# Kernel tuning notes

Measured on AMD Instinct MI355X. Metric: run time of the kernel, lower is better.

Reference implementation:

```python
import jax, jax.numpy as jnp
import numpy as np

T, N, E, D = 4, 50000, 800000, 256
VOCAB = 64000


def _gcn_layer(x, row, col, w, W, b, n):
    # PyG GCNConv: add self-loops (weight 1), symmetric normalization on
    # weighted in-degree (target/col), h = x @ W, scatter-add, then + bias.
    loops = jnp.arange(n, dtype=row.dtype)
    row2 = jnp.concatenate([row, loops])
    col2 = jnp.concatenate([col, loops])
    w2 = jnp.concatenate([w, jnp.ones((n,), x.dtype)])
    deg = jax.ops.segment_sum(w2, col2, num_segments=n)
    dinv = jnp.where(deg > 0, jax.lax.rsqrt(deg), 0.0)
    norm = dinv[row2] * w2 * dinv[col2]              # [E+N]
    h = x @ W                                        # [N, D]
    out = jax.ops.segment_sum(norm[:, None] * h[row2], col2, num_segments=n)
    return out + b


def _encode_timestep(ids, row, col, w, emb, W1, b1, W2, b2, W3, b3):
    x = emb[ids]                                     # [N, D] embedding lookup
    x = _gcn_layer(x, row, col, w, W1, b1, ids.shape[0])
    x = _gcn_layer(x, row, col, w, W2, b2, ids.shape[0])
    x = _gcn_layer(x, row, col, w, W3, b3, ids.shape[0])
    return x


def setup_inputs() -> dict:
    key = jax.random.key(0)
    ks = jax.random.split(key, 8)
    scale = 1.0 / np.sqrt(D)
    return {
        "node_features": jax.random.randint(ks[0], (T, N), 0, VOCAB, dtype=jnp.int32),
        "edge_index": jax.random.randint(ks[1], (T, 2, E), 0, N, dtype=jnp.int32),
        "edge_weight": jax.random.uniform(ks[2], (T, E), dtype=jnp.float32),
        "emb": jax.random.normal(ks[3], (VOCAB, D), dtype=jnp.float32),
        "W1": jax.random.normal(ks[4], (D, D), dtype=jnp.float32) * scale,
        "b1": jnp.zeros((D,), jnp.float32),
        "W2": jax.random.normal(ks[5], (D, D), dtype=jnp.float32) * scale,
        "b2": jnp.zeros((D,), jnp.float32),
        "W3": jax.random.normal(ks[6], (D, D), dtype=jnp.float32) * scale,
        "b3": jnp.zeros((D,), jnp.float32),
    }


def reference(node_features, edge_index, edge_weight, emb, W1, b1, W2, b2, W3, b3):
    outs = []
    for t in range(node_features.shape[0]):  # fixed small timestep count
        outs.append(_encode_timestep(node_features[t], edge_index[t, 0],
                                     edge_index[t, 1], edge_weight[t],
                                     emb, W1, b1, W2, b2, W3, b3))
    return jnp.concatenate(outs, axis=0)  # [T*N, D]
```

## Files before the change

kernel.cpp:

```cpp
#include <hip/hip_runtime.h>

#define T_STEPS 4
#define NN 50000
#define EE 800000
#define DD 256
#define NB ((NN + 255) / 256)

typedef __attribute__((ext_vector_type(8))) short short8;
typedef __attribute__((ext_vector_type(4))) float floatx4;

__device__ __forceinline__ unsigned short f2bf(float f) {
    unsigned u = __float_as_uint(f);
    return (unsigned short)((u + 0x7FFFu + ((u >> 16) & 1u)) >> 16);
}
__device__ __forceinline__ float bf2f(unsigned short s) {
    return __uint_as_float(((unsigned)s) << 16);
}

__device__ __forceinline__ void async16(const unsigned short* g, unsigned short* l) {
    __builtin_amdgcn_global_load_lds(
        (const __attribute__((address_space(1))) void*)g,
        (__attribute__((address_space(3))) void*)l, 16, 0, 0);
}

__global__ __launch_bounds__(256) void init_deg_cnt(float* __restrict__ deg,
                                                    int* __restrict__ cnt, int n) {
    int i = blockIdx.x * 256 + threadIdx.x;
    if (i < n) { deg[i] = 1.0f; cnt[i] = 0; }
}

__global__ __launch_bounds__(256) void edge_deg_cnt(const int* __restrict__ col,
                                                    const float* __restrict__ w,
                                                    float* __restrict__ deg,
                                                    int* __restrict__ cnt, int e) {
    int i = blockIdx.x * 256 + threadIdx.x;
    if (i < e) {
        int c = col[i];
        atomicAdd(&deg[c], w[i]);
        atomicAdd(&cnt[c], 1);
    }
}

__global__ __launch_bounds__(256) void compute_dinv(const float* __restrict__ deg,
                                                    float* __restrict__ dinv, int n) {
    int i = blockIdx.x * 256 + threadIdx.x;
    if (i < n) {
        float d = deg[i];
        dinv[i] = d > 0.0f ? rsqrtf(d) : 0.0f;
    }
}

__global__ __launch_bounds__(256) void block_sums(const int* __restrict__ cnt,
                                                  int* __restrict__ bsum, int n) {
    __shared__ int sm[256];
    int i = blockIdx.x * 256 + threadIdx.x;
    sm[threadIdx.x] = (i < n) ? cnt[i] : 0;
    __syncthreads();
    for (int s = 128; s > 0; s >>= 1) {
        if ((int)threadIdx.x < s) sm[threadIdx.x] += sm[threadIdx.x + s];
        __syncthreads();
    }
    if (threadIdx.x == 0) bsum[blockIdx.x] = sm[0];
}

__global__ __launch_bounds__(256) void scan_bsum(const int* __restrict__ bsum,
                                                 int* __restrict__ boff, int nb) {
    __shared__ int sm[256];
    int v = ((int)threadIdx.x < nb) ? bsum[threadIdx.x] : 0;
    sm[threadIdx.x] = v;
    __syncthreads();
    for (int o = 1; o < 256; o <<= 1) {
        int t = (threadIdx.x >= (unsigned)o) ? sm[threadIdx.x - o] : 0;
        __syncthreads();
        sm[threadIdx.x] += t;
        __syncthreads();
    }
    if ((int)threadIdx.x < nb) boff[threadIdx.x] = sm[threadIdx.x] - v;
}

__global__ __launch_bounds__(256) void scan_final(const int* __restrict__ cnt,
                                                  const int* __restrict__ boff,
                                                  int* __restrict__ colptr,
                                                  int* __restrict__ next, int n, int e) {
    __shared__ int sm[256];
    int i = blockIdx.x * 256 + threadIdx.x;
    int v = (i < n) ? cnt[i] : 0;
    sm[threadIdx.x] = v;
    __syncthreads();
    for (int o = 1; o < 256; o <<= 1) {
        int t = (threadIdx.x >= (unsigned)o) ? sm[threadIdx.x - o] : 0;
        __syncthreads();
        sm[threadIdx.x] += t;
        __syncthreads();
    }
    int excl = sm[threadIdx.x] - v + boff[blockIdx.x];
    if (i < n) { colptr[i] = excl; next[i] = excl; }
    if (i == 0) colptr[n] = e;
}

__global__ __launch_bounds__(256) void fill_csr(const int* __restrict__ row,
                                                const int* __restrict__ col,
                                                const float* __restrict__ w,
                                                const float* __restrict__ dinv,
                                                int* __restrict__ next,
                                                int* __restrict__ srow,
                                                float* __restrict__ snorm, int e) {
    int i = blockIdx.x * 256 + threadIdx.x;
    if (i < e) {
        int r = row[i], c = col[i];
        int p = atomicAdd(&next[c], 1);
        srow[p] = r;
        snorm[p] = dinv[r] * w[i] * dinv[c];
    }
}

__global__ __launch_bounds__(256) void convert_w(const float* __restrict__ W0,
                                                 const float* __restrict__ W1,
                                                 const float* __restrict__ W2,
                                                 unsigned short* __restrict__ wt) {
    int n = blockIdx.x;
    int k = threadIdx.x;
    int l = blockIdx.y;
    const float* W = (l == 0) ? W0 : (l == 1) ? W1 : W2;
    wt[(size_t)l * 65536 + n * 256 + k] = f2bf(W[k * 256 + n]);
}

__global__ __launch_bounds__(256) void embed_kernel(const int* __restrict__ ids,
                                                    const float* __restrict__ emb,
                                                    unsigned short* __restrict__ xb,
                                                    int n) {
    int t = blockIdx.x * 256 + threadIdx.x;
    if (t < n * 64) {
        int node = t >> 6;
        int j = t & 63;
        float4 v = ((const float4*)emb)[(size_t)ids[node] * 64 + j];
        ushort4 o;
        o.x = f2bf(v.x); o.y = f2bf(v.y); o.z = f2bf(v.z); o.w = f2bf(v.w);
        ((ushort4*)xb)[(size_t)node * 64 + j] = o;
    }
}

__global__ __launch_bounds__(256) void mfma_gemm(const unsigned short* __restrict__ xb,
                                                 const unsigned short* __restrict__ wt,
                                                 unsigned short* __restrict__ h2,
                                                 int M) {
    __shared__ __align__(16) unsigned short As[128 * 32];
    __shared__ __align__(16) unsigned short Bs[128 * 32];

    int tid = threadIdx.x;
    int lane = tid & 63;
    int wave = tid >> 6;
    int row0 = blockIdx.y * 128;
    int col0 = blockIdx.x * 128;
    int wm = (wave & 1) * 64;
    int wn = (wave >> 1) * 64;
    int quad = lane >> 4;
    int cl = lane & 15;

    int idx0 = tid, idx1 = 256 + tid;
    int c0 = idx0 >> 7, m0 = idx0 & 127;
    int c1 = idx1 >> 7, m1 = idx1 & 127;
    int gr0 = row0 + m0; if (gr0 >= M) gr0 = M - 1;
    int gr1 = row0 + m1; if (gr1 >= M) gr1 = M - 1;
    const unsigned short* srcA0 = xb + (size_t)gr0 * 256 + c0 * 8;
    const unsigned short* srcA1 = xb + (size_t)gr1 * 256 + c1 * 8;
    const unsigned short* srcB0 = wt + (size_t)(col0 + m0) * 256 + c0 * 8;
    const unsigned short* srcB1 = wt + (size_t)(col0 + m1) * 256 + c1 * 8;
    unsigned short* dstA0 = As + idx0 * 8;
    unsigned short* dstA1 = As + idx1 * 8;
    unsigned short* dstB0 = Bs + idx0 * 8;
    unsigned short* dstB1 = Bs + idx1 * 8;

    floatx4 acc[4][4] = {};

    for (int k0 = 0; k0 < 256; k0 += 32) {
        if (k0) __syncthreads();
        async16(srcA0 + k0, dstA0);
        async16(srcA1 + k0, dstA1);
        async16(srcB0 + k0, dstB0);
        async16(srcB1 + k0, dstB1);
        __syncthreads();

        short8 af[4], bfr[4];
#pragma unroll
        for (int i = 0; i < 4; ++i)
            af[i] = *(const short8*)&As[(quad * 128 + wm + i * 16 + cl) * 8];
#pragma unroll
        for (int j = 0; j < 4; ++j)
            bfr[j] = *(const short8*)&Bs[(quad * 128 + wn + j * 16 + cl) * 8];
#pragma unroll
        for (int i = 0; i < 4; ++i)
#pragma unroll
            for (int j = 0; j < 4; ++j)
                acc[i][j] = __builtin_amdgcn_mfma_f32_16x16x32_bf16(
                    af[i], bfr[j], acc[i][j], 0, 0, 0);
    }

#pragma unroll
    for (int i = 0; i < 4; ++i) {
#pragma unroll
        for (int r = 0; r < 4; ++r) {
            int gr = row0 + wm + i * 16 + quad * 4 + r;
            if (gr < M) {
                size_t base = (size_t)gr * 256 + col0 + wn + cl;
#pragma unroll
                for (int j = 0; j < 4; ++j)
                    h2[base + j * 16] = f2bf(acc[i][j][r]);
            }
        }
    }
}

__global__ __launch_bounds__(256) void agg_kernel(const unsigned short* __restrict__ h2,
                                                  const int* __restrict__ colptr,
                                                  const int* __restrict__ srow,
                                                  const float* __restrict__ snorm,
                                                  const float* __restrict__ dinv,
                                                  const float* __restrict__ bias,
                                                  float* __restrict__ dstf,
                                                  unsigned short* __restrict__ dstb,
                                                  int n) {
    int wave = threadIdx.x >> 6;
    int lane = threadIdx.x & 63;
    int c = blockIdx.x * 4 + wave;
    if (c >= n) return;
    int p0 = colptr[c];
    int p1 = colptr[c + 1];
    float di = dinv[c];
    float self = di * di;

    const ushort4* h4 = (const ushort4*)h2;
    int cbase = c * 64 + lane;

    ushort4 sv = h4[cbase];
    float ax = self * bf2f(sv.x), ay = self * bf2f(sv.y);
    float az = self * bf2f(sv.z), aw = self * bf2f(sv.w);
    float bx = 0.f, by = 0.f, bz = 0.f, bw = 0.f;

    int j = p0;
    for (; j + 1 < p1; j += 2) {
        int r0 = srow[j];
        int r1 = srow[j + 1];
        float w0 = snorm[j];
        float w1 = snorm[j + 1];
        ushort4 v0 = h4[(size_t)r0 * 64 + lane];
        ushort4 v1 = h4[(size_t)r1 * 64 + lane];
        ax += w0 * bf2f(v0.x); ay += w0 * bf2f(v0.y);
        az += w0 * bf2f(v0.z); aw += w0 * bf2f(v0.w);
        bx += w1 * bf2f(v1.x); by += w1 * bf2f(v1.y);
        bz += w1 * bf2f(v1.z); bw += w1 * bf2f(v1.w);
    }
    if (j < p1) {
        int r0 = srow[j];
        float w0 = snorm[j];
        ushort4 v0 = h4[(size_t)r0 * 64 + lane];
        ax += w0 * bf2f(v0.x); ay += w0 * bf2f(v0.y);
        az += w0 * bf2f(v0.z); aw += w0 * bf2f(v0.w);
    }
    float4 bv = ((const float4*)bias)[lane];
    float ox = ax + bx + bv.x, oy = ay + by + bv.y;
    float oz = az + bz + bv.z, ow = aw + bw + bv.w;
    if (dstb) {
        ushort4 o;
        o.x = f2bf(ox); o.y = f2bf(oy); o.z = f2bf(oz); o.w = f2bf(ow);
        ((ushort4*)dstb)[cbase] = o;
    } else {
        ((float4*)dstf)[cbase] = make_float4(ox, oy, oz, ow);
    }
}

extern "C" void kernel_launch(void* const* d_in, const int* in_sizes, int n_in,
                              void* d_out, int out_size, void* d_ws, size_t ws_size,
                              hipStream_t stream) {
    const int*   node_features = (const int*)d_in[0];
    const int*   edge_index    = (const int*)d_in[1];
    const float* edge_weight   = (const float*)d_in[2];
    const float* emb           = (const float*)d_in[3];
    const float* Wl[3] = {(const float*)d_in[4], (const float*)d_in[6], (const float*)d_in[8]};
    const float* bl[3] = {(const float*)d_in[5], (const float*)d_in[7], (const float*)d_in[9]};
    float* out = (float*)d_out;

    char* ws = (char*)d_ws;
    size_t off = 0;
    auto alloc = [&](size_t bytes) -> void* {
        void* p = ws + off;
        off = (off + bytes + 255) & ~(size_t)255;
        return p;
    };
    unsigned short* xb     = (unsigned short*)alloc((size_t)NN * DD * 2);
    unsigned short* h2     = (unsigned short*)alloc((size_t)NN * DD * 2);
    unsigned short* wt     = (unsigned short*)alloc((size_t)3 * DD * DD * 2);
    float* deg    = (float*)alloc((size_t)NN * 4);
    float* dinv   = (float*)alloc((size_t)NN * 4);
    int*   cnt    = (int*)alloc((size_t)NN * 4);
    int*   colptr = (int*)alloc((size_t)(NN + 1) * 4);
    int*   next   = (int*)alloc((size_t)NN * 4);
    int*   srow   = (int*)alloc((size_t)EE * 4);
    float* snorm  = (float*)alloc((size_t)EE * 4);
    int*   bsum   = (int*)alloc((size_t)NB * 4);
    int*   boff   = (int*)alloc((size_t)NB * 4);
    (void)ws_size; (void)n_in; (void)in_sizes; (void)out_size;

    const int gN   = (NN + 255) / 256;
    const int gE   = (EE + 255) / 256;
    const int gX   = (NN * 64 + 255) / 256;
    const int gAgg = (NN + 3) / 4;
    dim3 gGemm(2, (NN + 127) / 128);
    dim3 gCvt(256, 3);

    convert_w<<<gCvt, 256, 0, stream>>>(Wl[0], Wl[1], Wl[2], wt);

    for (int t = 0; t < T_STEPS; ++t) {
        const int*   ids = node_features + (size_t)t * NN;
        const int*   row = edge_index + (size_t)t * 2 * EE;
        const int*   col = row + EE;
        const float* w   = edge_weight + (size_t)t * EE;

        init_deg_cnt<<<gN, 256, 0, stream>>>(deg, cnt, NN);
        edge_deg_cnt<<<gE, 256, 0, stream>>>(col, w, deg, cnt, EE);
        compute_dinv<<<gN, 256, 0, stream>>>(deg, dinv, NN);
        block_sums<<<NB, 256, 0, stream>>>(cnt, bsum, NN);
        scan_bsum<<<1, 256, 0, stream>>>(bsum, boff, NB);
        scan_final<<<NB, 256, 0, stream>>>(cnt, boff, colptr, next, NN, EE);
        fill_csr<<<gE, 256, 0, stream>>>(row, col, w, dinv, next, srow, snorm, EE);

        embed_kernel<<<gX, 256, 0, stream>>>(ids, emb, xb, NN);

        for (int l = 0; l < 3; ++l) {
            mfma_gemm<<<gGemm, 256, 0, stream>>>(xb, wt + (size_t)l * DD * DD, h2, NN);
            if (l == 2) {
                agg_kernel<<<gAgg, 256, 0, stream>>>(h2, colptr, srow, snorm, dinv,
                                                     bl[l], out + (size_t)t * NN * DD,
                                                     nullptr, NN);
            } else {
                agg_kernel<<<gAgg, 256, 0, stream>>>(h2, colptr, srow, snorm, dinv,
                                                     bl[l], nullptr, xb, NN);
            }
        }
    }
}
```

Baseline: 1.944 ms.

## Collapse the three linear GCN layers into one GEMM and propagate biases analytically

Since the GCN layers have no nonlinearity, the three weight matrices are multiplied once into a combined W1·W2·W3. Each timestep then runs a single MFMA GEMM followed by three aggregation passes. The bias contributions are folded into the final aggregation using per-node propagated scalars (s1, s2) and precomputed vectors b1·W2·W3 and b2·W3. The embedding is converted to bf16 once, and the row gather is fused into the GEMM's A-tile loads, which removes the separate embed kernel. This cuts two GEMMs and one embed pass per timestep. In exchange it adds one full-vocabulary conversion, two small scalar-propagation kernels, and rounding from the product weight being stored in bf16.

```diff
diff --git a/kernel.cpp b/kernel.cpp
--- a/kernel.cpp
+++ b/kernel.cpp
@@ -4,6 +4,7 @@
 #define NN 50000
 #define EE 800000
 #define DD 256
+#define VOCAB 64000
 #define NB ((NN + 255) / 256)
 
 typedef __attribute__((ext_vector_type(8))) short short8;
@@ -114,33 +115,83 @@
     }
 }
 
-__global__ __launch_bounds__(256) void convert_w(const float* __restrict__ W0,
-                                                 const float* __restrict__ W1,
-                                                 const float* __restrict__ W2,
-                                                 unsigned short* __restrict__ wt) {
+__global__ __launch_bounds__(256) void s1_kernel(const int* __restrict__ colptr,
+                                                 const float* __restrict__ snorm,
+                                                 const float* __restrict__ dinv,
+                                                 float* __restrict__ s1, int n) {
+    int c = blockIdx.x * 256 + threadIdx.x;
+    if (c < n) {
+        float di = dinv[c];
+        float s = di * di;
+        int p1 = colptr[c + 1];
+        for (int p = colptr[c]; p < p1; ++p) s += snorm[p];
+        s1[c] = s;
+    }
+}
+
+__global__ __launch_bounds__(256) void s2_kernel(const int* __restrict__ colptr,
+                                                 const int* __restrict__ srow,
+                                                 const float* __restrict__ snorm,
+                                                 const float* __restrict__ dinv,
+                                                 const float* __restrict__ s1,
+                                                 float* __restrict__ s2, int n) {
+    int c = blockIdx.x * 256 + threadIdx.x;
+    if (c < n) {
+        float di = dinv[c];
+        float s = di * di * s1[c];
+        int p1 = colptr[c + 1];
+        for (int p = colptr[c]; p < p1; ++p) s += snorm[p] * s1[srow[p]];
+        s2[c] = s;
+    }
+}
+
+__global__ __launch_bounds__(256) void matmul256(const float* __restrict__ A,
+                                                 const float* __restrict__ B,
+                                                 float* __restrict__ C) {
+    __shared__ float arow[256];
+    int i = blockIdx.x, j = threadIdx.x;
+    arow[j] = A[i * 256 + j];
+    __syncthreads();
+    float acc = 0.f;
+#pragma unroll 8
+    for (int k = 0; k < 256; ++k) acc += arow[k] * B[k * 256 + j];
+    C[i * 256 + j] = acc;
+}
+
+__global__ __launch_bounds__(256) void matvec256(const float* __restrict__ x,
+                                                 const float* __restrict__ W,
+                                                 float* __restrict__ y) {
+    __shared__ float xs[256];
+    int j = threadIdx.x;
+    xs[j] = x[j];
+    __syncthreads();
+    float acc = 0.f;
+#pragma unroll 8
+    for (int k = 0; k < 256; ++k) acc += xs[k] * W[k * 256 + j];
+    y[j] = acc;
+}
+
+__global__ __launch_bounds__(256) void convert_wc(const float* __restrict__ Wc,
+                                                  unsigned short* __restrict__ wt) {
     int n = blockIdx.x;
     int k = threadIdx.x;
-    int l = blockIdx.y;
-    const float* W = (l == 0) ? W0 : (l == 1) ? W1 : W2;
-    wt[(size_t)l * 65536 + n * 256 + k] = f2bf(W[k * 256 + n]);
-}
-
-__global__ __launch_bounds__(256) void embed_kernel(const int* __restrict__ ids,
-                                                    const float* __restrict__ emb,
-                                                    unsigned short* __restrict__ xb,
-                                                    int n) {
+    wt[n * 256 + k] = f2bf(Wc[k * 256 + n]);
+}
+
+__global__ __launch_bounds__(256) void convert_emb(const float* __restrict__ emb,
+                                                   unsigned short* __restrict__ ebf,
+                                                   int total4) {
     int t = blockIdx.x * 256 + threadIdx.x;
-    if (t < n * 64) {
-        int node = t >> 6;
-        int j = t & 63;
-        float4 v = ((const float4*)emb)[(size_t)ids[node] * 64 + j];
+    if (t < total4) {
+        float4 v = ((const float4*)emb)[t];
         ushort4 o;
         o.x = f2bf(v.x); o.y = f2bf(v.y); o.z = f2bf(v.z); o.w = f2bf(v.w);
-        ((ushort4*)xb)[(size_t)node * 64 + j] = o;
-    }
-}
-
-__global__ __launch_bounds__(256) void mfma_gemm(const unsigned short* __restrict__ xb,
+        ((ushort4*)ebf)[t] = o;
+    }
+}
+
+__global__ __launch_bounds__(256) void mfma_gemm(const int* __restrict__ ids,
+                                                 const unsigned short* __restrict__ ebf,
                                                  const unsigned short* __restrict__ wt,
                                                  unsigned short* __restrict__ h2,
                                                  int M) {
@@ -159,13 +210,13 @@
 
     int idx0 = tid, idx1 = 256 + tid;
     int c0 = idx0 >> 7, m0 = idx0 & 127;
-    int c1 = idx1 >> 7, m1 = idx1 & 127;
+    int c1 = idx1 >> 7;
     int gr0 = row0 + m0; if (gr0 >= M) gr0 = M - 1;
-    int gr1 = row0 + m1; if (gr1 >= M) gr1 = M - 1;
-    const unsigned short* srcA0 = xb + (size_t)gr0 * 256 + c0 * 8;
-    const unsigned short* srcA1 = xb + (size_t)gr1 * 256 + c1 * 8;
+    int id0 = ids[gr0];
+    const unsigned short* srcA0 = ebf + (size_t)id0 * 256 + c0 * 8;
+    const unsigned short* srcA1 = ebf + (size_t)id0 * 256 + c1 * 8;
     const unsigned short* srcB0 = wt + (size_t)(col0 + m0) * 256 + c0 * 8;
-    const unsigned short* srcB1 = wt + (size_t)(col0 + m1) * 256 + c1 * 8;
+    const unsigned short* srcB1 = wt + (size_t)(col0 + m0) * 256 + c1 * 8;
     unsigned short* dstA0 = As + idx0 * 8;
     unsigned short* dstA1 = As + idx1 * 8;
     unsigned short* dstB0 = Bs + idx0 * 8;
@@ -216,7 +267,11 @@
                                                   const int* __restrict__ srow,
                                                   const float* __restrict__ snorm,
                                                   const float* __restrict__ dinv,
-                                                  const float* __restrict__ bias,
+                                                  const float* __restrict__ s1,
+                                                  const float* __restrict__ s2,
+                                                  const float* __restrict__ v1,
+                                                  const float* __restrict__ v2,
+                                                  const float* __restrict__ b3,
                                                   float* __restrict__ dstf,
                                                   unsigned short* __restrict__ dstb,
                                                   int n) {
@@ -244,11 +299,11 @@
         float w0 = snorm[j];
         float w1 = snorm[j + 1];
         ushort4 v0 = h4[(size_t)r0 * 64 + lane];
-        ushort4 v1 = h4[(size_t)r1 * 64 + lane];
+        ushort4 v1q = h4[(size_t)r1 * 64 + lane];
         ax += w0 * bf2f(v0.x); ay += w0 * bf2f(v0.y);
         az += w0 * bf2f(v0.z); aw += w0 * bf2f(v0.w);
-        bx += w1 * bf2f(v1.x); by += w1 * bf2f(v1.y);
-        bz += w1 * bf2f(v1.z); bw += w1 * bf2f(v1.w);
+        bx += w1 * bf2f(v1q.x); by += w1 * bf2f(v1q.y);
+        bz += w1 * bf2f(v1q.z); bw += w1 * bf2f(v1q.w);
     }
     if (j < p1) {
         int r0 = srow[j];
@@ -257,14 +312,20 @@
         ax += w0 * bf2f(v0.x); ay += w0 * bf2f(v0.y);
         az += w0 * bf2f(v0.z); aw += w0 * bf2f(v0.w);
     }
-    float4 bv = ((const float4*)bias)[lane];
-    float ox = ax + bx + bv.x, oy = ay + by + bv.y;
-    float oz = az + bz + bv.z, ow = aw + bw + bv.w;
+    float ox = ax + bx, oy = ay + by, oz = az + bz, ow = aw + bw;
     if (dstb) {
         ushort4 o;
         o.x = f2bf(ox); o.y = f2bf(oy); o.z = f2bf(oz); o.w = f2bf(ow);
         ((ushort4*)dstb)[cbase] = o;
     } else {
+        float s1c = s1[c], s2c = s2[c];
+        float4 a1 = ((const float4*)v1)[lane];
+        float4 a2 = ((const float4*)v2)[lane];
+        float4 a3 = ((const float4*)b3)[lane];
+        ox += s2c * a1.x + s1c * a2.x + a3.x;
+        oy += s2c * a1.y + s1c * a2.y + a3.y;
+        oz += s2c * a1.z + s1c * a2.z + a3.z;
+        ow += s2c * a1.w + s1c * a2.w + a3.w;
         ((float4*)dstf)[cbase] = make_float4(ox, oy, oz, ow);
     }
 }
@@ -276,8 +337,12 @@
     const int*   edge_index    = (const int*)d_in[1];
     const float* edge_weight   = (const float*)d_in[2];
     const float* emb           = (const float*)d_in[3];
-    const float* Wl[3] = {(const float*)d_in[4], (const float*)d_in[6], (const float*)d_in[8]};
-    const float* bl[3] = {(const float*)d_in[5], (const float*)d_in[7], (const float*)d_in[9]};
+    const float* W1 = (const float*)d_in[4];
+    const float* b1 = (const float*)d_in[5];
+    const float* W2 = (const float*)d_in[6];
+    const float* b2 = (const float*)d_in[7];
+    const float* W3 = (const float*)d_in[8];
+    const float* b3 = (const float*)d_in[9];
     float* out = (float*)d_out;
 
     char* ws = (char*)d_ws;
@@ -287,11 +352,19 @@
         off = (off + bytes + 255) & ~(size_t)255;
         return p;
     };
+    unsigned short* ebf    = (unsigned short*)alloc((size_t)VOCAB * DD * 2);
     unsigned short* xb     = (unsigned short*)alloc((size_t)NN * DD * 2);
     unsigned short* h2     = (unsigned short*)alloc((size_t)NN * DD * 2);
-    unsigned short* wt     = (unsigned short*)alloc((size_t)3 * DD * DD * 2);
+    unsigned short* wtc    = (unsigned short*)alloc((size_t)DD * DD * 2);
+    float* Wtmp   = (float*)alloc((size_t)DD * DD * 4);
+    float* Wc32   = (float*)alloc((size_t)DD * DD * 4);
+    float* u      = (float*)alloc((size_t)DD * 4);
+    float* v1     = (float*)alloc((size_t)DD * 4);
+    float* v2     = (float*)alloc((size_t)DD * 4);
     float* deg    = (float*)alloc((size_t)NN * 4);
     float* dinv   = (float*)alloc((size_t)NN * 4);
+    float* s1v    = (float*)alloc((size_t)NN * 4);
+    float* s2v    = (float*)alloc((size_t)NN * 4);
     int*   cnt    = (int*)alloc((size_t)NN * 4);
     int*   colptr = (int*)alloc((size_t)(NN + 1) * 4);
     int*   next   = (int*)alloc((size_t)NN * 4);
@@ -303,12 +376,17 @@
 
     const int gN   = (NN + 255) / 256;
     const int gE   = (EE + 255) / 256;
-    const int gX   = (NN * 64 + 255) / 256;
     const int gAgg = (NN + 3) / 4;
+    const int gEmb = (VOCAB * 64 + 255) / 256;
     dim3 gGemm(2, (NN + 127) / 128);
-    dim3 gCvt(256, 3);
-
-    convert_w<<<gCvt, 256, 0, stream>>>(Wl[0], Wl[1], Wl[2], wt);
+
+    convert_emb<<<gEmb, 256, 0, stream>>>(emb, ebf, VOCAB * 64);
+    matmul256<<<256, 256, 0, stream>>>(W1, W2, Wtmp);
+    matmul256<<<256, 256, 0, stream>>>(Wtmp, W3, Wc32);
+    convert_wc<<<256, 256, 0, stream>>>(Wc32, wtc);
+    matvec256<<<1, 256, 0, stream>>>(b1, W2, u);
+    matvec256<<<1, 256, 0, stream>>>(u, W3, v1);
+    matvec256<<<1, 256, 0, stream>>>(b2, W3, v2);
 
     for (int t = 0; t < T_STEPS; ++t) {
         const int*   ids = node_features + (size_t)t * NN;
@@ -324,18 +402,19 @@
         scan_final<<<NB, 256, 0, stream>>>(cnt, boff, colptr, next, NN, EE);
         fill_csr<<<gE, 256, 0, stream>>>(row, col, w, dinv, next, srow, snorm, EE);
 
-        embed_kernel<<<gX, 256, 0, stream>>>(ids, emb, xb, NN);
-
-        for (int l = 0; l < 3; ++l) {
-            mfma_gemm<<<gGemm, 256, 0, stream>>>(xb, wt + (size_t)l * DD * DD, h2, NN);
-            if (l == 2) {
-                agg_kernel<<<gAgg, 256, 0, stream>>>(h2, colptr, srow, snorm, dinv,
-                                                     bl[l], out + (size_t)t * NN * DD,
-                                                     nullptr, NN);
-            } else {
-                agg_kernel<<<gAgg, 256, 0, stream>>>(h2, colptr, srow, snorm, dinv,
-                                                     bl[l], nullptr, xb, NN);
-            }
-        }
-    }
-}
+        s1_kernel<<<gN, 256, 0, stream>>>(colptr, snorm, dinv, s1v, NN);
+        s2_kernel<<<gN, 256, 0, stream>>>(colptr, srow, snorm, dinv, s1v, s2v, NN);
+
+        mfma_gemm<<<gGemm, 256, 0, stream>>>(ids, ebf, wtc, h2, NN);
+
+        agg_kernel<<<gAgg, 256, 0, stream>>>(h2, colptr, srow, snorm, dinv,
+                                             nullptr, nullptr, nullptr, nullptr, nullptr,
+                                             nullptr, xb, NN);
+        agg_kernel<<<gAgg, 256, 0, stream>>>(xb, colptr, srow, snorm, dinv,
+                                             nullptr, nullptr, nullptr, nullptr, nullptr,
+                                             nullptr, h2, NN);
+        agg_kernel<<<gAgg, 256, 0, stream>>>(h2, colptr, srow, snorm, dinv,
+                                             s1v, s2v, v1, v2, b3,
+                                             out + (size_t)t * NN * DD, nullptr, NN);
+    }
+}
```

After: 1.798 ms. -7.5%, faster.
